# Optimization experiments

Hardware: AMD Instinct MI355X
Metric: run time of the kernel (lower is better)

Reference implementation:

```python
import jax, jax.numpy as jnp
import numpy as np

S, X, G = 2048, 2048, 2
INPUT_SIZE = (3, 32, 32)
F = int(np.prod(INPUT_SIZE))


def setup_inputs() -> dict:
    key = jax.random.key(0)
    k1, k2, k3 = jax.random.split(key, 3)
    samples = jax.random.normal(k1, (S,) + INPUT_SIZE, dtype=jnp.float32)
    x = jax.random.normal(k2, (X,) + INPUT_SIZE, dtype=jnp.float32)
    # per-feature std per gradation, kept in [0.1, 1.0) like ranges_std scaling
    std = jax.random.uniform(k3, (G, F), dtype=jnp.float32, minval=0.1, maxval=1.0)
    return {"samples": samples, "x": x, "std": std}


def reference(samples, x, std):
    # samples: [S, C, H, W], x: [X, C, H, W], std: [G, F]
    G_, F_ = std.shape
    s = samples.reshape(samples.shape[0], F_)  # [S, F]
    xf = x.reshape(x.shape[0], F_)             # [X, F]
    w = 1.0 / (std * std)                       # [G, F] precision
    # per-gradation normalizer: -0.5*F*log(2pi) - sum_f log(std)
    const = -0.5 * F_ * jnp.log(2.0 * jnp.pi) - jnp.sum(jnp.log(std), axis=1)  # [G]
    # sum_f -0.5*((s-x)/std)^2 expanded: -0.5*(s^2 w - 2 s w x + x^2 w)
    A = jnp.einsum('sf,gf->gs', s * s, w)        # [G, S]
    C = jnp.einsum('xf,gf->gx', xf * xf, w)      # [G, X]
    B = jnp.einsum('sf,gf,xf->gsx', s, w, xf)    # [G, S, X] cross term
    logits = -0.5 * (A[:, :, None] - 2.0 * B + C[:, None, :]) + const[:, None, None]
    lp = jax.nn.logsumexp(logits, axis=2)        # over x (mixture components)
    lp = jax.nn.logsumexp(lp, axis=0)            # over gradations
    return lp - jnp.log(jnp.float32(x.shape[0] * G_))
```

## Files before the change

kernel.cpp:

```cpp
#include <hip/hip_runtime.h>
#include <math.h>

#define S_N 2048
#define X_N 2048
#define G_N 2
#define F_N 3072

#define TM 128
#define TN 128
#define BK 32

typedef __bf16 bf16;
typedef __bf16 bf16x4 __attribute__((ext_vector_type(4)));
typedef __bf16 bf16x8 __attribute__((ext_vector_type(8)));
typedef float f32x4 __attribute__((ext_vector_type(4)));

__global__ void k_const(const float* __restrict__ stdv, float* __restrict__ constg) {
  int g = blockIdx.x;
  int t = threadIdx.x;
  float s = 0.f;
  for (int f = t; f < F_N; f += 256) s += logf(stdv[g * F_N + f]);
  for (int o = 32; o; o >>= 1) s += __shfl_xor(s, o);
  __shared__ float red[4];
  int w = t >> 6, l = t & 63;
  if (l == 0) red[w] = s;
  __syncthreads();
  if (t == 0) {
    float tot = red[0] + red[1] + red[2] + red[3];
    constg[g] = -0.5f * (float)F_N * 1.8378770664093453f - tot;
  }
}

__global__ void k_prep(const float* __restrict__ samples, const float* __restrict__ xin,
                       const float* __restrict__ stdv,
                       bf16* __restrict__ U, bf16* __restrict__ V,
                       float* __restrict__ A, float* __restrict__ C) {
  int r = blockIdx.x;
  int t = threadIdx.x;
  bool isS = (r < S_N);
  const float* src = isS ? (samples + (size_t)r * F_N) : (xin + (size_t)(r - S_N) * F_N);
  float4 row[3];
#pragma unroll
  for (int j = 0; j < 3; ++j) row[j] = ((const float4*)src)[t + j * 256];

  __shared__ float red[4];
  int w = t >> 6, l = t & 63;

  for (int g = 0; g < G_N; ++g) {
    const float4* sd = (const float4*)(stdv + (size_t)g * F_N);
    bf16* dst = isS ? (U + ((size_t)g * S_N + r) * F_N)
                    : (V + ((size_t)g * X_N + (r - S_N)) * F_N);
    float acc = 0.f;
#pragma unroll
    for (int j = 0; j < 3; ++j) {
      float4 d = sd[t + j * 256];
      float u0 = row[j].x / d.x;
      float u1 = row[j].y / d.y;
      float u2 = row[j].z / d.z;
      float u3 = row[j].w / d.w;
      bf16x4 b;
      b[0] = (bf16)u0; b[1] = (bf16)u1; b[2] = (bf16)u2; b[3] = (bf16)u3;
      float f0 = (float)b[0], f1 = (float)b[1], f2 = (float)b[2], f3 = (float)b[3];
      acc += f0 * f0 + f1 * f1 + f2 * f2 + f3 * f3;
      ((bf16x4*)dst)[t + j * 256] = b;
    }
    for (int o = 32; o; o >>= 1) acc += __shfl_xor(acc, o);
    __syncthreads();
    if (l == 0) red[w] = acc;
    __syncthreads();
    if (t == 0) {
      float tot = red[0] + red[1] + red[2] + red[3];
      if (isS) A[(size_t)g * S_N + r] = tot;
      else     C[(size_t)g * X_N + (r - S_N)] = tot;
    }
  }
}

__global__ __launch_bounds__(512, 4) void k_gemm(const bf16* __restrict__ U, const bf16* __restrict__ V,
                                                 const float* __restrict__ A, const float* __restrict__ C,
                                                 float* __restrict__ logits) {
  __shared__ bf16 ldsA[TM * BK];
  __shared__ bf16 ldsB[TN * BK];

  int t = threadIdx.x;
  int g = blockIdx.z;
  int bm = blockIdx.y * TM;
  int bn = blockIdx.x * TN;

  const bf16* Ub = U + ((size_t)g * S_N + bm) * F_N;
  const bf16* Vb = V + ((size_t)g * X_N + bn) * F_N;

  int wave = t >> 6, lane = t & 63;
  int wm = wave & 1;
  int wn = wave >> 1;
  int r = lane & 15, q = lane >> 4;
  int sq = q ^ (r & 3);

  int row0 = t >> 2, gc0 = (t & 3) ^ (row0 & 3);
  const bf16* gA0 = Ub + (size_t)row0 * F_N + gc0 * 8;
  const bf16* gB0 = Vb + (size_t)row0 * F_N + gc0 * 8;
  bf16* lA0 = ldsA + t * 8;
  bf16* lB0 = ldsB + t * 8;

  f32x4 acc[4][2] = {};

  int abase = (wm * 64 + r) * BK + sq * 8;
  int bbase = (wn * 32 + r) * BK + sq * 8;

  for (int k0 = 0; k0 < F_N; k0 += BK) {
    __syncthreads();
    __builtin_amdgcn_global_load_lds((const __attribute__((address_space(1))) void*)(gA0 + k0),
                                     (__attribute__((address_space(3))) void*)lA0, 16, 0, 0);
    __builtin_amdgcn_global_load_lds((const __attribute__((address_space(1))) void*)(gB0 + k0),
                                     (__attribute__((address_space(3))) void*)lB0, 16, 0, 0);
    __syncthreads();

    bf16x8 af[4], bfr[2];
#pragma unroll
    for (int mi = 0; mi < 4; ++mi) af[mi] = *(const bf16x8*)(ldsA + abase + mi * 16 * BK);
#pragma unroll
    for (int ni = 0; ni < 2; ++ni) bfr[ni] = *(const bf16x8*)(ldsB + bbase + ni * 16 * BK);

#pragma unroll
    for (int mi = 0; mi < 4; ++mi)
#pragma unroll
      for (int ni = 0; ni < 2; ++ni)
        acc[mi][ni] = __builtin_amdgcn_mfma_f32_16x16x32_bf16(af[mi], bfr[ni], acc[mi][ni], 0, 0, 0);
  }

  const float* Ap = A + (size_t)g * S_N + bm + wm * 64;
  const float* Cp = C + (size_t)g * X_N + bn + wn * 32;
  float cv[2];
#pragma unroll
  for (int ni = 0; ni < 2; ++ni) cv[ni] = Cp[ni * 16 + r];
#pragma unroll
  for (int mi = 0; mi < 4; ++mi) {
#pragma unroll
    for (int i = 0; i < 4; ++i) {
      int rowl = wm * 64 + mi * 16 + q * 4 + i;
      float av = Ap[mi * 16 + q * 4 + i];
      float* orow = logits + ((size_t)g * S_N + bm + rowl) * X_N + bn + wn * 32;
#pragma unroll
      for (int ni = 0; ni < 2; ++ni)
        orow[ni * 16 + r] = acc[mi][ni][i] - 0.5f * (av + cv[ni]);
    }
  }
}

__global__ void k_lse(const float* __restrict__ logits, const float* __restrict__ constg,
                      float* __restrict__ out) {
  int s = blockIdx.x, t = threadIdx.x;
  float c0 = constg[0], c1 = constg[1];
  const float4* p0 = (const float4*)(logits + (size_t)s * X_N);
  const float4* p1 = (const float4*)(logits + ((size_t)S_N + s) * X_N);
  float4 v[4];
  v[0] = p0[t]; v[1] = p0[t + 256];
  v[2] = p1[t]; v[3] = p1[t + 256];
  v[0].x += c0; v[0].y += c0; v[0].z += c0; v[0].w += c0;
  v[1].x += c0; v[1].y += c0; v[1].z += c0; v[1].w += c0;
  v[2].x += c1; v[2].y += c1; v[2].z += c1; v[2].w += c1;
  v[3].x += c1; v[3].y += c1; v[3].z += c1; v[3].w += c1;

  float m = v[0].x;
#pragma unroll
  for (int j = 0; j < 4; ++j) {
    m = fmaxf(m, v[j].x); m = fmaxf(m, v[j].y);
    m = fmaxf(m, v[j].z); m = fmaxf(m, v[j].w);
  }
  for (int o = 32; o; o >>= 1) m = fmaxf(m, __shfl_xor(m, o));
  __shared__ float redm[4];
  __shared__ float reds[4];
  int w = t >> 6, l = t & 63;
  if (l == 0) redm[w] = m;
  __syncthreads();
  m = fmaxf(fmaxf(redm[0], redm[1]), fmaxf(redm[2], redm[3]));

  float sum = 0.f;
#pragma unroll
  for (int j = 0; j < 4; ++j) {
    sum += expf(v[j].x - m) + expf(v[j].y - m) + expf(v[j].z - m) + expf(v[j].w - m);
  }
  for (int o = 32; o; o >>= 1) sum += __shfl_xor(sum, o);
  if (l == 0) reds[w] = sum;
  __syncthreads();
  if (t == 0) {
    float tot = reds[0] + reds[1] + reds[2] + reds[3];
    out[s] = m + logf(tot) - 8.317766166719343f;
  }
}

extern "C" void kernel_launch(void* const* d_in, const int* in_sizes, int n_in,
                              void* d_out, int out_size, void* d_ws, size_t ws_size,
                              hipStream_t stream) {
  const float* samples = (const float*)d_in[0];
  const float* xin     = (const float*)d_in[1];
  const float* stdv    = (const float*)d_in[2];
  float* out = (float*)d_out;

  char* ws = (char*)d_ws;
  size_t off = 0;
  bf16* U = (bf16*)(ws + off);       off += (size_t)G_N * S_N * F_N * 2;
  bf16* V = (bf16*)(ws + off);       off += (size_t)G_N * X_N * F_N * 2;
  float* logits = (float*)(ws + off); off += (size_t)G_N * S_N * X_N * 4;
  float* A = (float*)(ws + off);     off += (size_t)G_N * S_N * 4;
  float* C = (float*)(ws + off);     off += (size_t)G_N * X_N * 4;
  float* constg = (float*)(ws + off); off += 256;

  k_const<<<dim3(G_N), dim3(256), 0, stream>>>(stdv, constg);
  k_prep<<<dim3(S_N + X_N), dim3(256), 0, stream>>>(samples, xin, stdv, U, V, A, C);
  k_gemm<<<dim3(X_N / TN, S_N / TM, G_N), dim3(512), 0, stream>>>(U, V, A, C, logits);
  k_lse<<<dim3(S_N), dim3(256), 0, stream>>>(logits, constg, out);
}
```

Before: 180.7 us.

## Split-K GEMM with double-buffered LDS and move bias terms into LSE

The GEMM now splits the reduction dimension into two halves across grid z, doubling the block count. It double-buffers the LDS tiles so the next tile's global-to-LDS load is issued before the current tile's MFMAs, cutting one barrier per iteration. The LDS swizzle is changed and the occupancy hint raised to 8. The two partial products are written as separate fp32 buffers, and the A/C/const bias terms are added in the LSE kernel while it sums the partials. In exchange, fp32 intermediate traffic doubles on both the write side and the read side.

```diff
diff --git a/kernel.cpp b/kernel.cpp
--- a/kernel.cpp
+++ b/kernel.cpp
@@ -9,6 +9,8 @@
 #define TM 128
 #define TN 128
 #define BK 32
+#define KH (F_N / 2)
+#define ITERS (KH / BK)
 
 typedef __bf16 bf16;
 typedef __bf16 bf16x4 __attribute__((ext_vector_type(4)));
@@ -76,50 +78,55 @@
   }
 }
 
-__global__ __launch_bounds__(512, 4) void k_gemm(const bf16* __restrict__ U, const bf16* __restrict__ V,
-                                                 const float* __restrict__ A, const float* __restrict__ C,
-                                                 float* __restrict__ logits) {
-  __shared__ bf16 ldsA[TM * BK];
-  __shared__ bf16 ldsB[TN * BK];
+__global__ __launch_bounds__(512, 8) void k_gemm(const bf16* __restrict__ U, const bf16* __restrict__ V,
+                                                 float* __restrict__ parts) {
+  __shared__ bf16 ldsA[2][TM * BK];
+  __shared__ bf16 ldsB[2][TN * BK];
 
   int t = threadIdx.x;
-  int g = blockIdx.z;
+  int z = blockIdx.z;
+  int g = z >> 1, ks = z & 1;
   int bm = blockIdx.y * TM;
   int bn = blockIdx.x * TN;
 
-  const bf16* Ub = U + ((size_t)g * S_N + bm) * F_N;
-  const bf16* Vb = V + ((size_t)g * X_N + bn) * F_N;
+  const bf16* Ub = U + ((size_t)g * S_N + bm) * F_N + ks * KH;
+  const bf16* Vb = V + ((size_t)g * X_N + bn) * F_N + ks * KH;
 
   int wave = t >> 6, lane = t & 63;
   int wm = wave & 1;
   int wn = wave >> 1;
   int r = lane & 15, q = lane >> 4;
-  int sq = q ^ (r & 3);
-
-  int row0 = t >> 2, gc0 = (t & 3) ^ (row0 & 3);
+  int sq = q ^ ((r >> 1) & 3);
+
+  int row0 = t >> 2, cc = t & 3;
+  int gc0 = cc ^ ((row0 >> 1) & 3);
   const bf16* gA0 = Ub + (size_t)row0 * F_N + gc0 * 8;
   const bf16* gB0 = Vb + (size_t)row0 * F_N + gc0 * 8;
-  bf16* lA0 = ldsA + t * 8;
-  bf16* lB0 = ldsB + t * 8;
 
   f32x4 acc[4][2] = {};
-
   int abase = (wm * 64 + r) * BK + sq * 8;
   int bbase = (wn * 32 + r) * BK + sq * 8;
 
-  for (int k0 = 0; k0 < F_N; k0 += BK) {
+  __builtin_amdgcn_global_load_lds((const __attribute__((address_space(1))) void*)gA0,
+                                   (__attribute__((address_space(3))) void*)(&ldsA[0][t * 8]), 16, 0, 0);
+  __builtin_amdgcn_global_load_lds((const __attribute__((address_space(1))) void*)gB0,
+                                   (__attribute__((address_space(3))) void*)(&ldsB[0][t * 8]), 16, 0, 0);
+
+  for (int it = 0; it < ITERS; ++it) {
     __syncthreads();
-    __builtin_amdgcn_global_load_lds((const __attribute__((address_space(1))) void*)(gA0 + k0),
-                                     (__attribute__((address_space(3))) void*)lA0, 16, 0, 0);
-    __builtin_amdgcn_global_load_lds((const __attribute__((address_space(1))) void*)(gB0 + k0),
-                                     (__attribute__((address_space(3))) void*)lB0, 16, 0, 0);
-    __syncthreads();
+    int b = it & 1;
+    int nb = b ^ 1;
+    int nk = (it + 1) * BK;
+    __builtin_amdgcn_global_load_lds((const __attribute__((address_space(1))) void*)(gA0 + nk),
+                                     (__attribute__((address_space(3))) void*)(&ldsA[nb][t * 8]), 16, 0, 0);
+    __builtin_amdgcn_global_load_lds((const __attribute__((address_space(1))) void*)(gB0 + nk),
+                                     (__attribute__((address_space(3))) void*)(&ldsB[nb][t * 8]), 16, 0, 0);
 
     bf16x8 af[4], bfr[2];
 #pragma unroll
-    for (int mi = 0; mi < 4; ++mi) af[mi] = *(const bf16x8*)(ldsA + abase + mi * 16 * BK);
-#pragma unroll
-    for (int ni = 0; ni < 2; ++ni) bfr[ni] = *(const bf16x8*)(ldsB + bbase + ni * 16 * BK);
+    for (int mi = 0; mi < 4; ++mi) af[mi] = *(const bf16x8*)(&ldsA[b][abase + mi * 16 * BK]);
+#pragma unroll
+    for (int ni = 0; ni < 2; ++ni) bfr[ni] = *(const bf16x8*)(&ldsB[b][bbase + ni * 16 * BK]);
 
 #pragma unroll
     for (int mi = 0; mi < 4; ++mi)
@@ -128,38 +135,49 @@
         acc[mi][ni] = __builtin_amdgcn_mfma_f32_16x16x32_bf16(af[mi], bfr[ni], acc[mi][ni], 0, 0, 0);
   }
 
-  const float* Ap = A + (size_t)g * S_N + bm + wm * 64;
-  const float* Cp = C + (size_t)g * X_N + bn + wn * 32;
-  float cv[2];
-#pragma unroll
-  for (int ni = 0; ni < 2; ++ni) cv[ni] = Cp[ni * 16 + r];
+  float* P = parts + ((size_t)(ks * G_N + g) * S_N + bm) * X_N + bn;
 #pragma unroll
   for (int mi = 0; mi < 4; ++mi) {
 #pragma unroll
     for (int i = 0; i < 4; ++i) {
       int rowl = wm * 64 + mi * 16 + q * 4 + i;
-      float av = Ap[mi * 16 + q * 4 + i];
-      float* orow = logits + ((size_t)g * S_N + bm + rowl) * X_N + bn + wn * 32;
+      float* orow = P + (size_t)rowl * X_N + wn * 32;
 #pragma unroll
       for (int ni = 0; ni < 2; ++ni)
-        orow[ni * 16 + r] = acc[mi][ni][i] - 0.5f * (av + cv[ni]);
+        orow[ni * 16 + r] = acc[mi][ni][i];
     }
   }
 }
 
-__global__ void k_lse(const float* __restrict__ logits, const float* __restrict__ constg,
-                      float* __restrict__ out) {
+__global__ void k_lse(const float* __restrict__ parts,
+                      const float* __restrict__ A, const float* __restrict__ C,
+                      const float* __restrict__ constg, float* __restrict__ out) {
   int s = blockIdx.x, t = threadIdx.x;
-  float c0 = constg[0], c1 = constg[1];
-  const float4* p0 = (const float4*)(logits + (size_t)s * X_N);
-  const float4* p1 = (const float4*)(logits + ((size_t)S_N + s) * X_N);
-  float4 v[4];
-  v[0] = p0[t]; v[1] = p0[t + 256];
-  v[2] = p1[t]; v[3] = p1[t + 256];
-  v[0].x += c0; v[0].y += c0; v[0].z += c0; v[0].w += c0;
-  v[1].x += c0; v[1].y += c0; v[1].z += c0; v[1].w += c0;
-  v[2].x += c1; v[2].y += c1; v[2].z += c1; v[2].w += c1;
-  v[3].x += c1; v[3].y += c1; v[3].z += c1; v[3].w += c1;
+  float c0 = constg[0] - 0.5f * A[s];
+  float c1 = constg[1] - 0.5f * A[S_N + s];
+  const float4* p00 = (const float4*)(parts + (size_t)(0 * G_N + 0) * S_N * X_N + (size_t)s * X_N);
+  const float4* p01 = (const float4*)(parts + (size_t)(0 * G_N + 1) * S_N * X_N + (size_t)s * X_N);
+  const float4* p10 = (const float4*)(parts + (size_t)(1 * G_N + 0) * S_N * X_N + (size_t)s * X_N);
+  const float4* p11 = (const float4*)(parts + (size_t)(1 * G_N + 1) * S_N * X_N + (size_t)s * X_N);
+  const float4* Cg0 = (const float4*)(C);
+  const float4* Cg1 = (const float4*)(C + X_N);
+
+  float4 v[4], ca[4];
+  {
+    float4 a0 = p00[t], b0 = p10[t];
+    float4 a1 = p00[t + 256], b1 = p10[t + 256];
+    float4 a2 = p01[t], b2 = p11[t];
+    float4 a3 = p01[t + 256], b3 = p11[t + 256];
+    ca[0] = Cg0[t]; ca[1] = Cg0[t + 256]; ca[2] = Cg1[t]; ca[3] = Cg1[t + 256];
+    v[0].x = a0.x + b0.x + c0 - 0.5f * ca[0].x; v[0].y = a0.y + b0.y + c0 - 0.5f * ca[0].y;
+    v[0].z = a0.z + b0.z + c0 - 0.5f * ca[0].z; v[0].w = a0.w + b0.w + c0 - 0.5f * ca[0].w;
+    v[1].x = a1.x + b1.x + c0 - 0.5f * ca[1].x; v[1].y = a1.y + b1.y + c0 - 0.5f * ca[1].y;
+    v[1].z = a1.z + b1.z + c0 - 0.5f * ca[1].z; v[1].w = a1.w + b1.w + c0 - 0.5f * ca[1].w;
+    v[2].x = a2.x + b2.x + c1 - 0.5f * ca[2].x; v[2].y = a2.y + b2.y + c1 - 0.5f * ca[2].y;
+    v[2].z = a2.z + b2.z + c1 - 0.5f * ca[2].z; v[2].w = a2.w + b2.w + c1 - 0.5f * ca[2].w;
+    v[3].x = a3.x + b3.x + c1 - 0.5f * ca[3].x; v[3].y = a3.y + b3.y + c1 - 0.5f * ca[3].y;
+    v[3].z = a3.z + b3.z + c1 - 0.5f * ca[3].z; v[3].w = a3.w + b3.w + c1 - 0.5f * ca[3].w;
+  }
 
   float m = v[0].x;
 #pragma unroll
@@ -199,15 +217,15 @@
 
   char* ws = (char*)d_ws;
   size_t off = 0;
-  bf16* U = (bf16*)(ws + off);       off += (size_t)G_N * S_N * F_N * 2;
-  bf16* V = (bf16*)(ws + off);       off += (size_t)G_N * X_N * F_N * 2;
-  float* logits = (float*)(ws + off); off += (size_t)G_N * S_N * X_N * 4;
-  float* A = (float*)(ws + off);     off += (size_t)G_N * S_N * 4;
-  float* C = (float*)(ws + off);     off += (size_t)G_N * X_N * 4;
+  bf16* U = (bf16*)(ws + off);        off += (size_t)G_N * S_N * F_N * 2;
+  bf16* V = (bf16*)(ws + off);        off += (size_t)G_N * X_N * F_N * 2;
+  float* parts = (float*)(ws + off);  off += (size_t)2 * G_N * S_N * X_N * 4;
+  float* A = (float*)(ws + off);      off += (size_t)G_N * S_N * 4;
+  float* C = (float*)(ws + off);      off += (size_t)G_N * X_N * 4;
   float* constg = (float*)(ws + off); off += 256;
 
   k_const<<<dim3(G_N), dim3(256), 0, stream>>>(stdv, constg);
   k_prep<<<dim3(S_N + X_N), dim3(256), 0, stream>>>(samples, xin, stdv, U, V, A, C);
-  k_gemm<<<dim3(X_N / TN, S_N / TM, G_N), dim3(512), 0, stream>>>(U, V, A, C, logits);
-  k_lse<<<dim3(S_N), dim3(256), 0, stream>>>(logits, constg, out);
-}
+  k_gemm<<<dim3(X_N / TN, S_N / TM, 2 * G_N), dim3(512), 0, stream>>>(U, V, parts);
+  k_lse<<<dim3(S_N), dim3(256), 0, stream>>>(parts, A, C, constg, out);
+}
```

Measured after the change: 199.1 us. 1.1x slower.
